# Optimization experiments

Hardware: AMD Instinct MI355X
Metric: run time of the kernel (lower is better)

The kernel has to match this reference:

```python
import jax, jax.numpy as jnp
import numpy as np
from jax import lax

SEQ, BATCH, IN, HID, OUT = 168, 4096, 24, 64, 9


def _uniform(key, shape, scale):
    return jax.random.uniform(key, shape, jnp.float32, -scale, scale)


def setup_inputs() -> dict:
    key = jax.random.key(0)
    ks = jax.random.split(key, 12)
    s = 1.0 / np.sqrt(HID)  # PyTorch LSTM/Linear init scale
    return {
        "x": jax.random.normal(ks[0], (SEQ, BATCH, IN), jnp.float32),
        # layer 0 LSTM (PyTorch gate order: i, f, g, o stacked along dim 0)
        "W_ih0": _uniform(ks[1], (4 * HID, IN), s),
        "W_hh0": _uniform(ks[2], (4 * HID, HID), s),
        "b_ih0": _uniform(ks[3], (4 * HID,), s),
        "b_hh0": _uniform(ks[4], (4 * HID,), s),
        # layer 1 LSTM
        "W_ih1": _uniform(ks[5], (4 * HID, HID), s),
        "W_hh1": _uniform(ks[6], (4 * HID, HID), s),
        "b_ih1": _uniform(ks[7], (4 * HID,), s),
        "b_hh1": _uniform(ks[8], (4 * HID,), s),
        # linear head
        "W_out": _uniform(ks[9], (OUT, HID), s),
        "b_out": _uniform(ks[10], (OUT,), s),
    }


def _lstm_layer(x, W_ih, W_hh, b_ih, b_hh):
    # x: [S, B, D]; returns hidden states [S, B, H]
    H = W_hh.shape[1]
    B = x.shape[1]
    # precompute input projections for all timesteps: [S, B, 4H]
    xg = jnp.einsum('sbd,gd->sbg', x, W_ih) + b_ih + b_hh

    def step(carry, xg_t):
        h, c = carry
        g = xg_t + h @ W_hh.T  # [B, 4H]
        i, f, gc, o = jnp.split(g, 4, axis=-1)
        c = jax.nn.sigmoid(f) * c + jax.nn.sigmoid(i) * jnp.tanh(gc)
        h = jax.nn.sigmoid(o) * jnp.tanh(c)
        return (h, c), h

    init = (jnp.zeros((B, H), x.dtype), jnp.zeros((B, H), x.dtype))
    _, hs = lax.scan(step, init, xg)
    return hs


def reference(x, W_ih0, W_hh0, b_ih0, b_hh0, W_ih1, W_hh1, b_ih1, b_hh1, W_out, b_out):
    h = _lstm_layer(x, W_ih0, W_hh0, b_ih0, b_hh0)   # [S, B, H]
    h = _lstm_layer(h, W_ih1, W_hh1, b_ih1, b_hh1)   # [S, B, H]
    out = jnp.einsum('sbh,oh->sbo', h, W_out) + b_out  # [S, B, OUT]
    return out
```

## Files before the change

kernel.cpp:

```cpp
#include <hip/hip_runtime.h>
#include <hip/hip_bf16.h>
#include <math.h>

#define SEQ   168
#define BATCH 4096
#define NOUT  9
#define NBLK  256

typedef short bf16x8 __attribute__((ext_vector_type(8)));
typedef float f32x4  __attribute__((ext_vector_type(4)));

#define MFMA(a,b,c) __builtin_amdgcn_mfma_f32_16x16x32_bf16((a),(b),(c),0,0,0)

static __device__ __forceinline__ float bf2f(unsigned short h){
    unsigned int u = ((unsigned int)h) << 16;
    return __builtin_bit_cast(float, u);
}
static __device__ __forceinline__ unsigned short f2bf(float f){
    return __builtin_bit_cast(unsigned short, __float2bfloat16(f));
}
static __device__ __forceinline__ void splitf(float f, unsigned short& hi, unsigned short& lo){
    hi = f2bf(f);
    float r = f - bf2f(hi);
    lo = (unsigned short)(__builtin_bit_cast(unsigned int, r) >> 16);
}
static __device__ __forceinline__ float sigf(float x){
    return __builtin_amdgcn_rcpf(1.0f + __expf(-x));
}
static __device__ __forceinline__ float tanhf_(float x){
    float r = __builtin_amdgcn_rcpf(1.0f + __expf(2.0f * x));
    return fmaf(-2.0f, r, 1.0f);
}
static __device__ __forceinline__ bf16x8 ldfrag(const unsigned short* p){
    const uint4 q = *reinterpret_cast<const uint4*>(p);
    return __builtin_bit_cast(bf16x8, q);
}

static __device__ __forceinline__ void gbar(int* cnt, int* phs, int* done,
                                            int tickval, int& ph, int lane){
    asm volatile("s_waitcnt lgkmcnt(0)" ::: "memory");
    if (lane == 0){
        int old = __hip_atomic_fetch_add(cnt, 1, __ATOMIC_ACQ_REL,
                                         __HIP_MEMORY_SCOPE_WORKGROUP);
        if (old == 3){
            *cnt = 0;
            __hip_atomic_store(done, tickval, __ATOMIC_RELEASE,
                               __HIP_MEMORY_SCOPE_WORKGROUP);
            __hip_atomic_store(phs, ph ^ 1, __ATOMIC_RELEASE,
                               __HIP_MEMORY_SCOPE_WORKGROUP);
        }
    }
    while (__hip_atomic_load(phs, __ATOMIC_ACQUIRE,
                             __HIP_MEMORY_SCOPE_WORKGROUP) == ph)
        __builtin_amdgcn_s_sleep(1);
    ph ^= 1;
}
static __device__ __forceinline__ void wait_ge(int* done, int need){
    if (__hip_atomic_load(done, __ATOMIC_ACQUIRE, __HIP_MEMORY_SCOPE_WORKGROUP) >= need) return;
    do { __builtin_amdgcn_s_sleep(1); }
    while (__hip_atomic_load(done, __ATOMIC_ACQUIRE, __HIP_MEMORY_SCOPE_WORKGROUP) < need);
}

__global__ __launch_bounds__(512, 2)
void lstm_fused(const float* __restrict__ x,
                const float* __restrict__ Wih0, const float* __restrict__ Whh0,
                const float* __restrict__ bih0, const float* __restrict__ bhh0,
                const float* __restrict__ Wih1, const float* __restrict__ Whh1,
                const float* __restrict__ bih1, const float* __restrict__ bhh1,
                const float* __restrict__ Wout, const float* __restrict__ bout,
                float* __restrict__ out)
{
    __shared__ __align__(16) unsigned short sXH[2][16][72];
    __shared__ __align__(16) unsigned short sH0H[3][16][72];
    __shared__ __align__(16) unsigned short sH1H[2][16][72];
    __shared__ int sync[8];

    const int tid  = threadIdx.x;
    const int half = tid >> 8;
    const int w2   = (tid >> 6) & 3;
    const int l    = tid & 63;
    const int lr   = l & 15;
    const int g    = l >> 4;
    const int r0   = blockIdx.x * 16;
    const int cg   = w2 * 16 + lr;

    if (tid < 8) sync[tid] = (tid == 4) ? -1 : 0;

    for (int i = tid; i < (int)(2*16*72/2); i += 512){
        ((unsigned int*)sXH)[i]  = 0u;
        ((unsigned int*)sH1H)[i] = 0u;
    }
    for (int i = tid; i < (int)(3*16*72/2); i += 512)
        ((unsigned int*)sH0H)[i] = 0u;
    __syncthreads();
    if (tid < 96){
        const float4 v = *reinterpret_cast<const float4*>(&x[(size_t)r0 * 24 + tid * 4]);
        const int row = (tid * 4) / 24, col = (tid * 4) % 24;
        ushort4 w = { f2bf(v.x), f2bf(v.y), f2bf(v.z), f2bf(v.w) };
        *reinterpret_cast<ushort4*>(&sXH[0][row][col]) = w;
    }
    __syncthreads();

    if (half == 0){
        bf16x8 B0H[4][3], B0L[4][3];
        #pragma unroll
        for (int gt = 0; gt < 4; ++gt){
            const int c = gt * 64 + cg;
            bf16x8 bh = {0,0,0,0,0,0,0,0}, bl = {0,0,0,0,0,0,0,0};
            if (g < 3){
                const float* pw = &Wih0[c * 24 + g * 8];
                #pragma unroll
                for (int j = 0; j < 8; ++j){ unsigned short hh, ll; splitf(pw[j], hh, ll); bh[j]=(short)hh; bl[j]=(short)ll; }
            }
            B0H[gt][0] = bh; B0L[gt][0] = bl;
            #pragma unroll
            for (int ks = 0; ks < 2; ++ks){
                bf16x8 ch, cl;
                const float* pw = &Whh0[c * 64 + ks * 32 + g * 8];
                #pragma unroll
                for (int j = 0; j < 8; ++j){ unsigned short hh, ll; splitf(pw[j], hh, ll); ch[j]=(short)hh; cl[j]=(short)ll; }
                B0H[gt][1+ks] = ch; B0L[gt][1+ks] = cl;
            }
        }
        float b0[4];
        #pragma unroll
        for (int gt = 0; gt < 4; ++gt) b0[gt] = bih0[gt*64 + cg] + bhh0[gt*64 + cg];

        const float* xfp = x + ((size_t)BATCH + r0) * 24 + tid * 4;
        float c0[4] = {0,0,0,0};
        int ph = 0;
        int pw = 0, pr = 2;
        for (int t = 0; t < SEQ; ++t){
            const int px = t & 1;
            const bool ldx = (tid < 96) && (t + 1 < SEQ);
            float4 pref;
            if (ldx){ pref = *reinterpret_cast<const float4*>(xfp); xfp += (size_t)BATCH * 24; }

            const bf16x8 AxH = ldfrag(&sXH[px][lr][g*8]);
            bf16x8 A0H[2];
            #pragma unroll
            for (int ks = 0; ks < 2; ++ks)
                A0H[ks] = ldfrag(&sH0H[pr][lr][ks*32 + g*8]);

            f32x4 a0[4];
            #pragma unroll
            for (int gt = 0; gt < 4; ++gt){ f32x4 a = {b0[gt],b0[gt],b0[gt],b0[gt]}; a0[gt] = a; }
            #pragma unroll
            for (int gt = 0; gt < 4; ++gt) a0[gt] = MFMA(AxH, B0H[gt][0], a0[gt]);
            #pragma unroll
            for (int gt = 0; gt < 4; ++gt) a0[gt] = MFMA(AxH, B0L[gt][0], a0[gt]);
            #pragma unroll
            for (int ks = 0; ks < 2; ++ks){
                #pragma unroll
                for (int gt = 0; gt < 4; ++gt) a0[gt] = MFMA(A0H[ks], B0H[gt][1+ks], a0[gt]);
                #pragma unroll
                for (int gt = 0; gt < 4; ++gt) a0[gt] = MFMA(A0H[ks], B0L[gt][1+ks], a0[gt]);
            }
            unsigned short hh[4];
            #pragma unroll
            for (int i = 0; i < 4; ++i){
                const float ig = sigf(a0[0][i]);
                const float fg = sigf(a0[1][i]);
                const float gg = tanhf_(a0[2][i]);
                const float og = sigf(a0[3][i]);
                c0[i] = fg * c0[i] + ig * gg;
                hh[i] = f2bf(og * tanhf_(c0[i]));
            }
            if (t >= 3) wait_ge(&sync[5], t - 2);
            #pragma unroll
            for (int i = 0; i < 4; ++i)
                sH0H[pw][g * 4 + i][cg] = hh[i];
            if (ldx){
                const int row = (tid * 4) / 24, col = (tid * 4) % 24;
                ushort4 w = { f2bf(pref.x), f2bf(pref.y), f2bf(pref.z), f2bf(pref.w) };
                *reinterpret_cast<ushort4*>(&sXH[px ^ 1][row][col]) = w;
            }
            gbar(&sync[0], &sync[2], &sync[4], t, ph, l);
            pw = (pw == 2) ? 0 : pw + 1;
            pr = (pr == 2) ? 0 : pr + 1;
        }
    } else {
        bf16x8 B1H[4][4], B1L[4][4];
        #pragma unroll
        for (int gt = 0; gt < 4; ++gt){
            const int c = gt * 64 + cg;
            #pragma unroll
            for (int ks = 0; ks < 2; ++ks){
                bf16x8 ch, cl;
                const float* pw = &Wih1[c * 64 + ks * 32 + g * 8];
                #pragma unroll
                for (int j = 0; j < 8; ++j){ unsigned short hh, ll; splitf(pw[j], hh, ll); ch[j]=(short)hh; cl[j]=(short)ll; }
                B1H[gt][ks] = ch; B1L[gt][ks] = cl;
            }
            #pragma unroll
            for (int ks = 0; ks < 2; ++ks){
                bf16x8 ch, cl;
                const float* pw = &Whh1[c * 64 + ks * 32 + g * 8];
                #pragma unroll
                for (int j = 0; j < 8; ++j){ unsigned short hh, ll; splitf(pw[j], hh, ll); ch[j]=(short)hh; cl[j]=(short)ll; }
                B1H[gt][2+ks] = ch; B1L[gt][2+ks] = cl;
            }
        }
        float b1[4];
        #pragma unroll
        for (int gt = 0; gt < 4; ++gt) b1[gt] = bih1[gt*64 + cg] + bhh1[gt*64 + cg];

        const int oc = lr;
        bf16x8 WoH[2], WoL[2];
        #pragma unroll
        for (int tt = 0; tt < 2; ++tt){
            bf16x8 bh = {0,0,0,0,0,0,0,0}, bl = {0,0,0,0,0,0,0,0};
            if (oc < NOUT){
                const float* pw = &Wout[oc * 64 + tt * 32 + g * 8];
                #pragma unroll
                for (int j = 0; j < 8; ++j){ unsigned short hh, ll; splitf(pw[j], hh, ll); bh[j]=(short)hh; bl[j]=(short)ll; }
            }
            WoH[tt] = bh; WoL[tt] = bl;
        }
        const float bo0 = (oc < NOUT) ? bout[oc] : 0.f;
        float* houtp = out + (size_t)(r0 + g * 4) * NOUT + oc;

        float c1[4] = {0,0,0,0};
        int ph = 0;
        int pr0 = 0;
        for (int t = 1; t <= SEQ; ++t){
            const int p = t & 1;
            bf16x8 A1H[2];
            #pragma unroll
            for (int ks = 0; ks < 2; ++ks)
                A1H[ks] = ldfrag(&sH1H[p][lr][ks*32 + g*8]);
            wait_ge(&sync[4], t - 1);
            bf16x8 A0H[2];
            #pragma unroll
            for (int ks = 0; ks < 2; ++ks)
                A0H[ks] = ldfrag(&sH0H[pr0][lr][ks*32 + g*8]);

            f32x4 a1[4];
            #pragma unroll
            for (int gt = 0; gt < 4; ++gt){ f32x4 a = {b1[gt],b1[gt],b1[gt],b1[gt]}; a1[gt] = a; }
            #pragma unroll
            for (int ks = 0; ks < 2; ++ks){
                #pragma unroll
                for (int gt = 0; gt < 4; ++gt) a1[gt] = MFMA(A1H[ks], B1H[gt][2+ks], a1[gt]);
                #pragma unroll
                for (int gt = 0; gt < 4; ++gt) a1[gt] = MFMA(A1H[ks], B1L[gt][2+ks], a1[gt]);
            }
            if (t >= 2 && w2 == (t & 3)){
                f32x4 ha = {bo0, bo0, bo0, bo0};
                ha = MFMA(A1H[0], WoH[0], ha);
                ha = MFMA(A1H[0], WoL[0], ha);
                ha = MFMA(A1H[1], WoH[1], ha);
                ha = MFMA(A1H[1], WoL[1], ha);
                if (oc < NOUT){
                    #pragma unroll
                    for (int i = 0; i < 4; ++i)
                        houtp[(size_t)i * NOUT] = ha[i];
                }
            }
            if (t >= 2) houtp += (size_t)BATCH * NOUT;
            #pragma unroll
            for (int ks = 0; ks < 2; ++ks){
                #pragma unroll
                for (int gt = 0; gt < 4; ++gt) a1[gt] = MFMA(A0H[ks], B1H[gt][ks], a1[gt]);
                #pragma unroll
                for (int gt = 0; gt < 4; ++gt) a1[gt] = MFMA(A0H[ks], B1L[gt][ks], a1[gt]);
            }
            #pragma unroll
            for (int i = 0; i < 4; ++i){
                const float ig = sigf(a1[0][i]);
                const float fg = sigf(a1[1][i]);
                const float gg = tanhf_(a1[2][i]);
                const float og = sigf(a1[3][i]);
                c1[i] = fg * c1[i] + ig * gg;
                sH1H[p ^ 1][g * 4 + i][cg] = f2bf(og * tanhf_(c1[i]));
            }
            gbar(&sync[1], &sync[3], &sync[5], t, ph, l);
            pr0 = (pr0 == 2) ? 0 : pr0 + 1;
        }
        {
            const int pe = (SEQ + 1) & 1;
            if (w2 == ((SEQ + 1) & 3)){
                bf16x8 A1H0 = ldfrag(&sH1H[pe][lr][g*8]);
                bf16x8 A1H1 = ldfrag(&sH1H[pe][lr][32 + g*8]);
                f32x4 ha = {bo0, bo0, bo0, bo0};
                ha = MFMA(A1H0, WoH[0], ha);
                ha = MFMA(A1H0, WoL[0], ha);
                ha = MFMA(A1H1, WoH[1], ha);
                ha = MFMA(A1H1, WoL[1], ha);
                if (oc < NOUT){
                    #pragma unroll
                    for (int i = 0; i < 4; ++i)
                        houtp[(size_t)i * NOUT] = ha[i];
                }
            }
        }
    }
}

extern "C" void kernel_launch(void* const* d_in, const int* in_sizes, int n_in,
                              void* d_out, int out_size, void* d_ws, size_t ws_size,
                              hipStream_t stream)
{
    const float* x    = (const float*)d_in[0];
    const float* Wih0 = (const float*)d_in[1];
    const float* Whh0 = (const float*)d_in[2];
    const float* bih0 = (const float*)d_in[3];
    const float* bhh0 = (const float*)d_in[4];
    const float* Wih1 = (const float*)d_in[5];
    const float* Whh1 = (const float*)d_in[6];
    const float* bih1 = (const float*)d_in[7];
    const float* bhh1 = (const float*)d_in[8];
    const float* Wout = (const float*)d_in[9];
    const float* bout = (const float*)d_in[10];
    float* out = (float*)d_out;

    lstm_fused<<<NBLK, 512, 0, stream>>>(x, Wih0, Whh0, bih0, bhh0,
                                         Wih1, Whh1, bih1, bhh1,
                                         Wout, bout, out);
}
```

Before: 186.8 us.

## Precompute next-step input projections off the recurrent critical path

Both LSTM layers now compute the input-projection MFMAs for the next timestep after the current gate activations, then carry them as a precomputed accumulator. The recurrent step only has to do the hidden-state MFMAs before the nonlinearities. The x staging buffer grows to three slots and prefetches two steps ahead. Layer 1 also waits on layer 0's output one step early, which reorders the cross-wave synchronisation. This adds register pressure and restructures the handoffs, which risks stalls or ordering errors.

```diff
diff --git a/kernel.cpp b/kernel.cpp
--- a/kernel.cpp
+++ b/kernel.cpp
@@ -70,7 +70,7 @@
                 const float* __restrict__ Wout, const float* __restrict__ bout,
                 float* __restrict__ out)
 {
-    __shared__ __align__(16) unsigned short sXH[2][16][72];
+    __shared__ __align__(16) unsigned short sXH[3][16][72];
     __shared__ __align__(16) unsigned short sH0H[3][16][72];
     __shared__ __align__(16) unsigned short sH1H[2][16][72];
     __shared__ int sync[8];
@@ -86,18 +86,21 @@
 
     if (tid < 8) sync[tid] = (tid == 4) ? -1 : 0;
 
-    for (int i = tid; i < (int)(2*16*72/2); i += 512){
+    for (int i = tid; i < (int)(3*16*72/2); i += 512){
         ((unsigned int*)sXH)[i]  = 0u;
+        ((unsigned int*)sH0H)[i] = 0u;
+    }
+    for (int i = tid; i < (int)(2*16*72/2); i += 512)
         ((unsigned int*)sH1H)[i] = 0u;
-    }
-    for (int i = tid; i < (int)(3*16*72/2); i += 512)
-        ((unsigned int*)sH0H)[i] = 0u;
     __syncthreads();
     if (tid < 96){
-        const float4 v = *reinterpret_cast<const float4*>(&x[(size_t)r0 * 24 + tid * 4]);
         const int row = (tid * 4) / 24, col = (tid * 4) % 24;
-        ushort4 w = { f2bf(v.x), f2bf(v.y), f2bf(v.z), f2bf(v.w) };
-        *reinterpret_cast<ushort4*>(&sXH[0][row][col]) = w;
+        const float4 v0 = *reinterpret_cast<const float4*>(&x[(size_t)r0 * 24 + tid * 4]);
+        const float4 v1 = *reinterpret_cast<const float4*>(&x[((size_t)BATCH + r0) * 24 + tid * 4]);
+        ushort4 w0 = { f2bf(v0.x), f2bf(v0.y), f2bf(v0.z), f2bf(v0.w) };
+        ushort4 w1 = { f2bf(v1.x), f2bf(v1.y), f2bf(v1.z), f2bf(v1.w) };
+        *reinterpret_cast<ushort4*>(&sXH[0][row][col]) = w0;
+        *reinterpret_cast<ushort4*>(&sXH[1][row][col]) = w1;
     }
     __syncthreads();
 
@@ -126,29 +129,33 @@
         #pragma unroll
         for (int gt = 0; gt < 4; ++gt) b0[gt] = bih0[gt*64 + cg] + bhh0[gt*64 + cg];
 
-        const float* xfp = x + ((size_t)BATCH + r0) * 24 + tid * 4;
+        f32x4 acc_pre[4];
+        {
+            const bf16x8 Ax = ldfrag(&sXH[0][lr][g*8]);
+            #pragma unroll
+            for (int gt = 0; gt < 4; ++gt){ f32x4 a = {b0[gt],b0[gt],b0[gt],b0[gt]}; acc_pre[gt] = a; }
+            #pragma unroll
+            for (int gt = 0; gt < 4; ++gt) acc_pre[gt] = MFMA(Ax, B0H[gt][0], acc_pre[gt]);
+            #pragma unroll
+            for (int gt = 0; gt < 4; ++gt) acc_pre[gt] = MFMA(Ax, B0L[gt][0], acc_pre[gt]);
+        }
+
+        const float* xfp = x + ((size_t)2 * BATCH + r0) * 24 + tid * 4;
         float c0[4] = {0,0,0,0};
         int ph = 0;
         int pw = 0, pr = 2;
+        int bxr = 1, bxw = 2;
         for (int t = 0; t < SEQ; ++t){
-            const int px = t & 1;
-            const bool ldx = (tid < 96) && (t + 1 < SEQ);
+            const bool ldx = (tid < 96) && (t + 2 < SEQ);
             float4 pref;
             if (ldx){ pref = *reinterpret_cast<const float4*>(xfp); xfp += (size_t)BATCH * 24; }
 
-            const bf16x8 AxH = ldfrag(&sXH[px][lr][g*8]);
             bf16x8 A0H[2];
-            #pragma unroll
-            for (int ks = 0; ks < 2; ++ks)
-                A0H[ks] = ldfrag(&sH0H[pr][lr][ks*32 + g*8]);
-
+            A0H[0] = ldfrag(&sH0H[pr][lr][g*8]);
+            A0H[1] = ldfrag(&sH0H[pr][lr][32 + g*8]);
             f32x4 a0[4];
             #pragma unroll
-            for (int gt = 0; gt < 4; ++gt){ f32x4 a = {b0[gt],b0[gt],b0[gt],b0[gt]}; a0[gt] = a; }
-            #pragma unroll
-            for (int gt = 0; gt < 4; ++gt) a0[gt] = MFMA(AxH, B0H[gt][0], a0[gt]);
-            #pragma unroll
-            for (int gt = 0; gt < 4; ++gt) a0[gt] = MFMA(AxH, B0L[gt][0], a0[gt]);
+            for (int gt = 0; gt < 4; ++gt) a0[gt] = acc_pre[gt];
             #pragma unroll
             for (int ks = 0; ks < 2; ++ks){
                 #pragma unroll
@@ -166,18 +173,29 @@
                 c0[i] = fg * c0[i] + ig * gg;
                 hh[i] = f2bf(og * tanhf_(c0[i]));
             }
-            if (t >= 3) wait_ge(&sync[5], t - 2);
-            #pragma unroll
-            for (int i = 0; i < 4; ++i)
-                sH0H[pw][g * 4 + i][cg] = hh[i];
+            if (t + 1 < SEQ){
+                const bf16x8 Axn = ldfrag(&sXH[bxr][lr][g*8]);
+                #pragma unroll
+                for (int gt = 0; gt < 4; ++gt){ f32x4 a = {b0[gt],b0[gt],b0[gt],b0[gt]}; acc_pre[gt] = a; }
+                #pragma unroll
+                for (int gt = 0; gt < 4; ++gt) acc_pre[gt] = MFMA(Axn, B0H[gt][0], acc_pre[gt]);
+                #pragma unroll
+                for (int gt = 0; gt < 4; ++gt) acc_pre[gt] = MFMA(Axn, B0L[gt][0], acc_pre[gt]);
+            }
             if (ldx){
                 const int row = (tid * 4) / 24, col = (tid * 4) % 24;
                 ushort4 w = { f2bf(pref.x), f2bf(pref.y), f2bf(pref.z), f2bf(pref.w) };
-                *reinterpret_cast<ushort4*>(&sXH[px ^ 1][row][col]) = w;
-            }
+                *reinterpret_cast<ushort4*>(&sXH[bxw][row][col]) = w;
+            }
+            if (t >= 3) wait_ge(&sync[5], t - 2);
+            #pragma unroll
+            for (int i = 0; i < 4; ++i)
+                sH0H[pw][g * 4 + i][cg] = hh[i];
             gbar(&sync[0], &sync[2], &sync[4], t, ph, l);
-            pw = (pw == 2) ? 0 : pw + 1;
-            pr = (pr == 2) ? 0 : pr + 1;
+            pr = pw;
+            pw  = (pw  == 2) ? 0 : pw  + 1;
+            bxr = (bxr == 2) ? 0 : bxr + 1;
+            bxw = (bxw == 2) ? 0 : bxw + 1;
         }
     } else {
         bf16x8 B1H[4][4], B1L[4][4];
@@ -220,30 +238,49 @@
         const float bo0 = (oc < NOUT) ? bout[oc] : 0.f;
         float* houtp = out + (size_t)(r0 + g * 4) * NOUT + oc;
 
+        f32x4 acc_pre[4];
+        {
+            wait_ge(&sync[4], 0);
+            bf16x8 A0H[2];
+            A0H[0] = ldfrag(&sH0H[0][lr][g*8]);
+            A0H[1] = ldfrag(&sH0H[0][lr][32 + g*8]);
+            #pragma unroll
+            for (int gt = 0; gt < 4; ++gt){ f32x4 a = {b1[gt],b1[gt],b1[gt],b1[gt]}; acc_pre[gt] = a; }
+            #pragma unroll
+            for (int ks = 0; ks < 2; ++ks){
+                #pragma unroll
+                for (int gt = 0; gt < 4; ++gt) acc_pre[gt] = MFMA(A0H[ks], B1H[gt][ks], acc_pre[gt]);
+                #pragma unroll
+                for (int gt = 0; gt < 4; ++gt) acc_pre[gt] = MFMA(A0H[ks], B1L[gt][ks], acc_pre[gt]);
+            }
+        }
+
         float c1[4] = {0,0,0,0};
         int ph = 0;
-        int pr0 = 0;
+        int pr0 = 1;
         for (int t = 1; t <= SEQ; ++t){
             const int p = t & 1;
             bf16x8 A1H[2];
-            #pragma unroll
-            for (int ks = 0; ks < 2; ++ks)
-                A1H[ks] = ldfrag(&sH1H[p][lr][ks*32 + g*8]);
-            wait_ge(&sync[4], t - 1);
-            bf16x8 A0H[2];
-            #pragma unroll
-            for (int ks = 0; ks < 2; ++ks)
-                A0H[ks] = ldfrag(&sH0H[pr0][lr][ks*32 + g*8]);
-
+            A1H[0] = ldfrag(&sH1H[p][lr][g*8]);
+            A1H[1] = ldfrag(&sH1H[p][lr][32 + g*8]);
             f32x4 a1[4];
             #pragma unroll
-            for (int gt = 0; gt < 4; ++gt){ f32x4 a = {b1[gt],b1[gt],b1[gt],b1[gt]}; a1[gt] = a; }
+            for (int gt = 0; gt < 4; ++gt) a1[gt] = acc_pre[gt];
             #pragma unroll
             for (int ks = 0; ks < 2; ++ks){
                 #pragma unroll
                 for (int gt = 0; gt < 4; ++gt) a1[gt] = MFMA(A1H[ks], B1H[gt][2+ks], a1[gt]);
                 #pragma unroll
                 for (int gt = 0; gt < 4; ++gt) a1[gt] = MFMA(A1H[ks], B1L[gt][2+ks], a1[gt]);
+            }
+            #pragma unroll
+            for (int i = 0; i < 4; ++i){
+                const float ig = sigf(a1[0][i]);
+                const float fg = sigf(a1[1][i]);
+                const float gg = tanhf_(a1[2][i]);
+                const float og = sigf(a1[3][i]);
+                c1[i] = fg * c1[i] + ig * gg;
+                sH1H[p ^ 1][g * 4 + i][cg] = f2bf(og * tanhf_(c1[i]));
             }
             if (t >= 2 && w2 == (t & 3)){
                 f32x4 ha = {bo0, bo0, bo0, bo0};
@@ -258,24 +295,23 @@
                 }
             }
             if (t >= 2) houtp += (size_t)BATCH * NOUT;
-            #pragma unroll
-            for (int ks = 0; ks < 2; ++ks){
-                #pragma unroll
-                for (int gt = 0; gt < 4; ++gt) a1[gt] = MFMA(A0H[ks], B1H[gt][ks], a1[gt]);
-                #pragma unroll
-                for (int gt = 0; gt < 4; ++gt) a1[gt] = MFMA(A0H[ks], B1L[gt][ks], a1[gt]);
-            }
-            #pragma unroll
-            for (int i = 0; i < 4; ++i){
-                const float ig = sigf(a1[0][i]);
-                const float fg = sigf(a1[1][i]);
-                const float gg = tanhf_(a1[2][i]);
-                const float og = sigf(a1[3][i]);
-                c1[i] = fg * c1[i] + ig * gg;
-                sH1H[p ^ 1][g * 4 + i][cg] = f2bf(og * tanhf_(c1[i]));
+            if (t < SEQ){
+                wait_ge(&sync[4], t);
+                bf16x8 A0H[2];
+                A0H[0] = ldfrag(&sH0H[pr0][lr][g*8]);
+                A0H[1] = ldfrag(&sH0H[pr0][lr][32 + g*8]);
+                #pragma unroll
+                for (int gt = 0; gt < 4; ++gt){ f32x4 a = {b1[gt],b1[gt],b1[gt],b1[gt]}; acc_pre[gt] = a; }
+                #pragma unroll
+                for (int ks = 0; ks < 2; ++ks){
+                    #pragma unroll
+                    for (int gt = 0; gt < 4; ++gt) acc_pre[gt] = MFMA(A0H[ks], B1H[gt][ks], acc_pre[gt]);
+                    #pragma unroll
+                    for (int gt = 0; gt < 4; ++gt) acc_pre[gt] = MFMA(A0H[ks], B1L[gt][ks], acc_pre[gt]);
+                }
+                pr0 = (pr0 == 2) ? 0 : pr0 + 1;
             }
             gbar(&sync[1], &sync[3], &sync[5], t, ph, l);
-            pr0 = (pr0 == 2) ? 0 : pr0 + 1;
         }
         {
             const int pe = (SEQ + 1) & 1;
```

New measurement: 213.7 us. 14.4% more time.
